# Optimization experiments

Measured on AMD Instinct MI355X. Metric: run time of the kernel, lower is better.

Reference implementation:

```python
import jax, jax.numpy as jnp
import numpy as np

N_NODES = 50000
N_EDGES = 1_600_000
DIMS = [3, 4096, 1024, 256, 64, 16]  # conv1..conv5 in/out widths


def setup_inputs() -> dict:
    key = jax.random.key(0)
    ks = jax.random.split(key, 2 + 2 * 6)
    x = jax.random.normal(ks[0], (N_NODES, DIMS[0]), jnp.float32)
    edge_index = jax.random.randint(ks[1], (2, N_EDGES), 0, N_NODES, jnp.int64)
    inp = {"x": x, "edge_index": edge_index}
    # GCNConv weights (lin has no bias fused; bias added after aggregation)
    for i in range(5):
        fi, fo = DIMS[i], DIMS[i + 1]
        inp[f"W{i+1}"] = jax.random.normal(ks[2 + 2 * i], (fi, fo), jnp.float32) / np.float32(np.sqrt(fi))
        inp[f"b{i+1}"] = jnp.zeros((fo,), jnp.float32)
    # final Linear(num_classes, 3)
    inp["Wl"] = jax.random.normal(ks[12], (DIMS[5], 3), jnp.float32) / np.float32(np.sqrt(DIMS[5]))
    inp["bl"] = jnp.zeros((3,), jnp.float32)
    return inp


def _gcn_layer(x, W, b, src, dst, dinv):
    """GCNConv: h = XW; out = D^-1/2 (A+I) D^-1/2 h + b (self-loops included)."""
    h = x @ W  # [N, out]
    norm = dinv[src] * dinv[dst]  # [E]
    agg = jax.ops.segment_sum(h[src] * norm[:, None], dst, num_segments=N_NODES)
    # self-loop term: norm_ii = dinv[i]^2
    return agg + h * (dinv * dinv)[:, None] + b


def reference(x, edge_index, W1, b1, W2, b2, W3, b3, W4, b4, W5, b5, Wl, bl):
    src, dst = edge_index[0], edge_index[1]
    # degree with self-loops (edge weights = 1), computed on target nodes
    deg = jax.ops.segment_sum(jnp.ones((N_EDGES,), x.dtype), dst, num_segments=N_NODES) + 1.0
    dinv = jax.lax.rsqrt(deg)
    h = _gcn_layer(x, W1, b1, src, dst, dinv)
    h = jax.nn.relu(h)  # dropout = identity in eval
    h = _gcn_layer(h, W2, b2, src, dst, dinv)
    h = jax.nn.relu(h)
    h = _gcn_layer(h, W3, b3, src, dst, dinv)
    h = jax.nn.relu(h)
    h = _gcn_layer(h, W4, b4, src, dst, dinv)
    h = jax.nn.relu(h)
    h = _gcn_layer(h, W5, b5, src, dst, dinv)
    # scatter_mean with broadcast index [0] -> global mean pool to [1, C]
    pooled = jnp.mean(h, axis=0, keepdims=True)
    return pooled @ Wl + bl  # [1, 3]
```

## Files before the change

### kernel.cpp

```cpp
#include <hip/hip_runtime.h>
#include <stdint.h>

#define NN 50000
#define NE 1600000

typedef _Float16 f16;
typedef __attribute__((ext_vector_type(8))) _Float16 h8;
typedef __attribute__((ext_vector_type(4))) _Float16 h4v;
typedef __attribute__((ext_vector_type(4))) float f32x4;
typedef __attribute__((ext_vector_type(2))) float f32x2;

union PackU { unsigned int u; f16 h[2]; };
union Pack4 { uint2 v; f16 h[4]; };

__device__ __forceinline__ void storev(float* p, float v) { *p = v; }
__device__ __forceinline__ void storev(f16* p, float v) { *p = (f16)v; }

__device__ __forceinline__ unsigned char f2fp8(float v) {
    int pk = __builtin_amdgcn_cvt_pk_fp8_f32(v, v, 0, false);
    return (unsigned char)(pk & 0xff);
}

__global__ __launch_bounds__(256) void zero_int_kernel(int* __restrict__ p, int n) {
    int i = blockIdx.x * 256 + threadIdx.x;
    if (i < n) p[i] = 0;
}

__global__ __launch_bounds__(256) void count_kernel(const int* __restrict__ dst,
                                                    int* __restrict__ deg, int nE) {
    int e = blockIdx.x * 256 + threadIdx.x;
    if (e < nE) atomicAdd(&deg[dst[e]], 1);
}

__global__ __launch_bounds__(256) void dinv_kernel(const int* __restrict__ deg,
                                                   float* __restrict__ dinv, int n) {
    int i = blockIdx.x * 256 + threadIdx.x;
    if (i < n) dinv[i] = rsqrtf((float)deg[i] + 1.0f);
}

__global__ __launch_bounds__(256) void scan1_kernel(const int* __restrict__ cnt,
                                                    int* __restrict__ rs,
                                                    int* __restrict__ bsum, int n) {
    __shared__ int sm[256];
    int b = blockIdx.x, t = threadIdx.x, i = b * 256 + t;
    int v = (i < n) ? cnt[i] : 0;
    sm[t] = v;
    __syncthreads();
    for (int off = 1; off < 256; off <<= 1) {
        int x = 0;
        if (t >= off) x = sm[t - off];
        __syncthreads();
        if (t >= off) sm[t] += x;
        __syncthreads();
    }
    if (i < n) rs[i] = sm[t] - v;
    if (t == 255) bsum[b] = sm[255];
}

__global__ __launch_bounds__(256) void scan2_kernel(int* __restrict__ bsum,
                                                    int* __restrict__ rs, int nb, int n) {
    __shared__ int sm[256];
    int t = threadIdx.x;
    int v = (t < nb) ? bsum[t] : 0;
    sm[t] = v;
    __syncthreads();
    for (int off = 1; off < 256; off <<= 1) {
        int x = 0;
        if (t >= off) x = sm[t - off];
        __syncthreads();
        if (t >= off) sm[t] += x;
        __syncthreads();
    }
    if (t < nb) bsum[t] = sm[t] - v;
    if (t == 255) rs[n] = sm[255];
}

__global__ __launch_bounds__(256) void scan3_kernel(int* __restrict__ rs,
                                                    const int* __restrict__ bsum, int n) {
    int i = blockIdx.x * 256 + threadIdx.x;
    if (i < n) rs[i] += bsum[blockIdx.x];
}

__global__ __launch_bounds__(256) void fill_kernel(const int* __restrict__ src,
                                                   const int* __restrict__ dst,
                                                   const int* __restrict__ rs,
                                                   int* __restrict__ cur,
                                                   int* __restrict__ csr, int nE) {
    int e = blockIdx.x * 256 + threadIdx.x;
    if (e < nE) {
        int d = dst[e];
        int p = rs[d] + atomicAdd(&cur[d], 1);
        csr[p] = src[e];
    }
}

__global__ __launch_bounds__(256) void pack_w1_kernel(const float* __restrict__ W1,
                                                      const float* __restrict__ b1,
                                                      float* __restrict__ w1p) {
    int k = blockIdx.x * 256 + threadIdx.x;
    if (k < 4096) {
        w1p[k * 4 + 0] = W1[k];
        w1p[k * 4 + 1] = W1[4096 + k];
        w1p[k * 4 + 2] = W1[8192 + k];
        w1p[k * 4 + 3] = b1[k];
    }
}

__global__ __launch_bounds__(256) void tconv_kernel(const float* __restrict__ W,
                                                    f16* __restrict__ Wt,
                                                    int K, int N) {
    __shared__ float tile[32][33];
    int kb = blockIdx.y * 32, nb = blockIdx.x * 32;
    int tx = threadIdx.x & 31, ty = threadIdx.x >> 5;
    for (int r = ty; r < 32; r += 8)
        tile[r][tx] = W[(size_t)(kb + r) * N + nb + tx];
    __syncthreads();
    for (int r = ty; r < 32; r += 8)
        Wt[(size_t)(nb + r) * K + kb + tx] = (f16)tile[tx][r];
}

template <int F, int TPN, bool RELU, bool BIAS, typename OutT>
__global__ __launch_bounds__(256) void agg_kernel(const float* __restrict__ t,
                                                  const float* __restrict__ dinv,
                                                  const int* __restrict__ rs,
                                                  const int* __restrict__ csr,
                                                  const float* __restrict__ bias,
                                                  OutT* __restrict__ out, int out_ld,
                                                  int nNodes) {
    constexpr int NPB = 256 / TPN;
    constexpr int C   = F / TPN;
    static_assert(TPN * C == F, "F must be TPN*C");
    int node = blockIdx.x * NPB + (int)threadIdx.x / TPN;
    if (node >= nNodes) return;
    int lane = (int)threadIdx.x % TPN;

    float acc[C];
#pragma unroll
    for (int c = 0; c < C; ++c) acc[c] = 0.f;

    int e0 = rs[node], e1 = rs[node + 1];
    for (int e = e0; e < e1; ++e) {
        int s = csr[e];
        float w = dinv[s];
        const float* tr = t + (size_t)s * F;
#pragma unroll
        for (int c = 0; c < C; ++c) acc[c] += w * tr[lane + c * TPN];
    }
    float di = dinv[node];
    const float* ti = t + (size_t)node * F;
    OutT* oi = out + (size_t)node * out_ld;
#pragma unroll
    for (int c = 0; c < C; ++c) {
        int col = lane + c * TPN;
        float v = di * acc[c] + di * di * ti[col];
        if (BIAS) v += bias[col];
        if (RELU) v = fmaxf(v, 0.f);
        storev(oi + col, v);
    }
}

template <bool RELU>
__global__ __launch_bounds__(256) void agg_fp8_256(const unsigned char* __restrict__ t,
                                                   int in_ld,
                                                   const float* __restrict__ dinv,
                                                   const int* __restrict__ rs,
                                                   const int* __restrict__ csr,
                                                   const float* __restrict__ bias,
                                                   f16* __restrict__ out,
                                                   int out_ld, int nNodes) {
    int node = blockIdx.x * 4 + ((int)threadIdx.x >> 6);
    if (node >= nNodes) return;
    int lane = (int)threadIdx.x & 63;

    float acc0 = 0.f, acc1 = 0.f, acc2 = 0.f, acc3 = 0.f;
    int e0 = rs[node], e1 = rs[node + 1];
    int e = e0;
    for (; e + 1 < e1; e += 2) {
        int s0 = csr[e], s1 = csr[e + 1];
        float w0 = dinv[s0], w1 = dinv[s1];
        unsigned int u0 = ((const unsigned int*)(t + (size_t)s0 * in_ld))[lane];
        unsigned int u1 = ((const unsigned int*)(t + (size_t)s1 * in_ld))[lane];
        f32x2 l0 = __builtin_amdgcn_cvt_pk_f32_fp8((int)u0, false);
        f32x2 h0 = __builtin_amdgcn_cvt_pk_f32_fp8((int)u0, true);
        f32x2 l1 = __builtin_amdgcn_cvt_pk_f32_fp8((int)u1, false);
        f32x2 h1 = __builtin_amdgcn_cvt_pk_f32_fp8((int)u1, true);
        acc0 += w0 * l0.x + w1 * l1.x;
        acc1 += w0 * l0.y + w1 * l1.y;
        acc2 += w0 * h0.x + w1 * h1.x;
        acc3 += w0 * h0.y + w1 * h1.y;
    }
    if (e < e1) {
        int s0 = csr[e];
        float w0 = dinv[s0];
        unsigned int u0 = ((const unsigned int*)(t + (size_t)s0 * in_ld))[lane];
        f32x2 l0 = __builtin_amdgcn_cvt_pk_f32_fp8((int)u0, false);
        f32x2 h0 = __builtin_amdgcn_cvt_pk_f32_fp8((int)u0, true);
        acc0 += w0 * l0.x;
        acc1 += w0 * l0.y;
        acc2 += w0 * h0.x;
        acc3 += w0 * h0.y;
    }
    float di = dinv[node], di2 = di * di;
    unsigned int us = ((const unsigned int*)(t + (size_t)node * in_ld))[lane];
    f32x2 sl = __builtin_amdgcn_cvt_pk_f32_fp8((int)us, false);
    f32x2 sh = __builtin_amdgcn_cvt_pk_f32_fp8((int)us, true);
    float4 b = *(const float4*)(bias + 4 * lane);
    float v0 = di * acc0 + di2 * sl.x + b.x;
    float v1 = di * acc1 + di2 * sl.y + b.y;
    float v2 = di * acc2 + di2 * sh.x + b.z;
    float v3 = di * acc3 + di2 * sh.y + b.w;
    if (RELU) {
        v0 = fmaxf(v0, 0.f); v1 = fmaxf(v1, 0.f);
        v2 = fmaxf(v2, 0.f); v3 = fmaxf(v3, 0.f);
    }
    Pack4 pk;
    pk.h[0] = (f16)v0; pk.h[1] = (f16)v1; pk.h[2] = (f16)v2; pk.h[3] = (f16)v3;
    *(uint2*)(out + (size_t)node * out_ld + 4 * lane) = pk.v;
}

#define LDSTR 40

__global__ __launch_bounds__(512, 4) void gemm12_mfma4(const float* __restrict__ aggx,
                                                       const float* __restrict__ w1p,
                                                       const f16* __restrict__ Bt,
                                                       unsigned char* __restrict__ t2) {
    __shared__ f16 As[128 * LDSTR] __attribute__((aligned(16)));
    __shared__ f16 Bs[256 * LDSTR] __attribute__((aligned(16)));
    int tid = threadIdx.x;
    int m0  = blockIdx.x * 128;
    int n0c = blockIdx.y * 256;

    int mg = tid >> 3;
    int kg = tid & 7;
    float a0[2], a1[2], a2[2];
#pragma unroll
    for (int j = 0; j < 2; ++j) {
        int gm = m0 + mg * 2 + j;
        if (gm < NN) {
            a0[j] = aggx[gm * 3 + 0];
            a1[j] = aggx[gm * 3 + 1];
            a2[j] = aggx[gm * 3 + 2];
        } else {
            a0[j] = a1[j] = a2[j] = 0.f;
        }
    }

    int brow = tid >> 1;
    int bkof = (tid & 1) * 16;
    const f16* bbase = Bt + (size_t)(n0c + brow) * 4096 + bkof;

    int lane   = tid & 63;
    int wv     = tid >> 6;
    int wm     = (wv >> 2) * 64;
    int wn     = (wv & 3) * 64;
    int fr_m   = lane & 15;
    int khalf8 = (lane >> 4) * 8;

    h8 pb0 = *(const h8*)(bbase);
    h8 pb1 = *(const h8*)(bbase + 8);

    f32x4 acc[4][4];
#pragma unroll
    for (int i = 0; i < 4; ++i)
#pragma unroll
        for (int j = 0; j < 4; ++j) acc[i][j] = (f32x4){0.f, 0.f, 0.f, 0.f};

    for (int k0 = 0; k0 < 4096; k0 += 32) {
        int kb = k0 + kg * 4;
        float4 wk0 = *(const float4*)(w1p + (size_t)(kb + 0) * 4);
        float4 wk1 = *(const float4*)(w1p + (size_t)(kb + 1) * 4);
        float4 wk2 = *(const float4*)(w1p + (size_t)(kb + 2) * 4);
        float4 wk3 = *(const float4*)(w1p + (size_t)(kb + 3) * 4);
#pragma unroll
        for (int j = 0; j < 2; ++j) {
            float h0 = fmaxf(a0[j] * wk0.x + a1[j] * wk0.y + a2[j] * wk0.z + wk0.w, 0.f);
            float h1 = fmaxf(a0[j] * wk1.x + a1[j] * wk1.y + a2[j] * wk1.z + wk1.w, 0.f);
            float h2 = fmaxf(a0[j] * wk2.x + a1[j] * wk2.y + a2[j] * wk2.z + wk2.w, 0.f);
            float h3 = fmaxf(a0[j] * wk3.x + a1[j] * wk3.y + a2[j] * wk3.z + wk3.w, 0.f);
            Pack4 pk;
            pk.h[0] = (f16)h0; pk.h[1] = (f16)h1; pk.h[2] = (f16)h2; pk.h[3] = (f16)h3;
            *(uint2*)(&As[(mg * 2 + j) * LDSTR + kg * 4]) = pk.v;
        }
        *(h8*)(&Bs[brow * LDSTR + bkof]) = pb0;
        *(h8*)(&Bs[brow * LDSTR + bkof + 8]) = pb1;
        __syncthreads();

        int kn = k0 + 32;
        if (kn < 4096) {
            pb0 = *(const h8*)(bbase + kn);
            pb1 = *(const h8*)(bbase + kn + 8);
        }

        h8 af[4];
#pragma unroll
        for (int mt = 0; mt < 4; ++mt)
            af[mt] = *(const h8*)(&As[(wm + mt * 16 + fr_m) * LDSTR + khalf8]);
#pragma unroll
        for (int nt = 0; nt < 4; ++nt) {
            h8 bf = *(const h8*)(&Bs[(wn + nt * 16 + fr_m) * LDSTR + khalf8]);
#pragma unroll
            for (int mt = 0; mt < 4; ++mt)
                acc[mt][nt] = __builtin_amdgcn_mfma_f32_16x16x32_f16(af[mt], bf, acc[mt][nt], 0, 0, 0);
        }
        __syncthreads();
    }

#pragma unroll
    for (int mt = 0; mt < 4; ++mt) {
#pragma unroll
        for (int reg = 0; reg < 4; ++reg) {
            int gm = m0 + wm + mt * 16 + (lane >> 4) * 4 + reg;
            if (gm < NN) {
                unsigned char* orow = t2 + (size_t)gm * 1024 + n0c + wn + fr_m;
#pragma unroll
                for (int nt = 0; nt < 4; ++nt)
                    orow[nt * 16] = f2fp8(acc[mt][nt][reg]);
            }
        }
    }
}

__global__ __launch_bounds__(256) void gemm_mfma(const f16* __restrict__ A, int lda,
                                                 const f16* __restrict__ Bt, int K,
                                                 unsigned char* __restrict__ C, int ldc,
                                                 int M) {
    __shared__ f16 As[128 * LDSTR] __attribute__((aligned(16)));
    __shared__ f16 Bs[128 * LDSTR] __attribute__((aligned(16)));
    int tid = threadIdx.x;
    int m0 = blockIdx.y * 128;
    int n0 = blockIdx.x * 128;

    int row = tid >> 1;
    int kof = (tid & 1) * 16;
    int am  = m0 + row;
    if (am > M - 1) am = M - 1;

    int lane   = tid & 63;
    int wv     = tid >> 6;
    int fr_m   = lane & 15;
    int khalf8 = (lane >> 4) * 8;

    const f16* abase = A + (size_t)am * lda + kof;
    const f16* bbase = Bt + (size_t)(n0 + row) * K + kof;

    h8 pa0 = *(const h8*)(abase);
    h8 pa1 = *(const h8*)(abase + 8);
    h8 pb0 = *(const h8*)(bbase);
    h8 pb1 = *(const h8*)(bbase + 8);

    f32x4 acc[2][8];
#pragma unroll
    for (int i = 0; i < 2; ++i)
#pragma unroll
        for (int j = 0; j < 8; ++j) acc[i][j] = (f32x4){0.f, 0.f, 0.f, 0.f};

    for (int k0 = 0; k0 < K; k0 += 32) {
        *(h8*)(&As[row * LDSTR + kof]) = pa0;
        *(h8*)(&As[row * LDSTR + kof + 8]) = pa1;
        *(h8*)(&Bs[row * LDSTR + kof]) = pb0;
        *(h8*)(&Bs[row * LDSTR + kof + 8]) = pb1;
        __syncthreads();

        int kn = k0 + 32;
        if (kn < K) {
            pa0 = *(const h8*)(abase + kn);
            pa1 = *(const h8*)(abase + kn + 8);
            pb0 = *(const h8*)(bbase + kn);
            pb1 = *(const h8*)(bbase + kn + 8);
        }

        h8 af0 = *(const h8*)(&As[(wv * 32 + fr_m) * LDSTR + khalf8]);
        h8 af1 = *(const h8*)(&As[(wv * 32 + 16 + fr_m) * LDSTR + khalf8]);
#pragma unroll
        for (int nt = 0; nt < 8; ++nt) {
            h8 bf = *(const h8*)(&Bs[(nt * 16 + fr_m) * LDSTR + khalf8]);
            acc[0][nt] = __builtin_amdgcn_mfma_f32_16x16x32_f16(af0, bf, acc[0][nt], 0, 0, 0);
            acc[1][nt] = __builtin_amdgcn_mfma_f32_16x16x32_f16(af1, bf, acc[1][nt], 0, 0, 0);
        }
        __syncthreads();
    }

#pragma unroll
    for (int mt = 0; mt < 2; ++mt) {
#pragma unroll
        for (int reg = 0; reg < 4; ++reg) {
            int gm = m0 + wv * 32 + mt * 16 + (lane >> 4) * 4 + reg;
            if (gm < M) {
                unsigned char* orow = C + (size_t)gm * ldc + n0 + fr_m;
#pragma unroll
                for (int nt = 0; nt < 8; ++nt)
                    orow[nt * 16] = f2fp8(acc[mt][nt][reg]);
            }
        }
    }
}

#define BM 64
#define BN 64
#define BKS 16
__global__ __launch_bounds__(256) void gemm_f16A_kernel(const f16* __restrict__ A,
                                                        const float* __restrict__ B,
                                                        float* __restrict__ C,
                                                        int M, int K, int N) {
    __shared__ float As[BKS][BM + 4];
    __shared__ float Bs[BKS][BN + 4];
    int tid = threadIdx.x;
    int tx = tid & 15;
    int ty = tid >> 4;
    int m0 = blockIdx.y * BM;
    int n0 = blockIdx.x * BN;

    float acc[4][4];
#pragma unroll
    for (int i = 0; i < 4; ++i)
#pragma unroll
        for (int j = 0; j < 4; ++j) acc[i][j] = 0.f;

    int lmA = tid >> 2;
    int lkA = (tid & 3) * 4;
    int lkB = tid >> 4;
    int lnB = (tid & 15) * 4;

    for (int k0 = 0; k0 < K; k0 += BKS) {
        int gm = m0 + lmA;
        if (gm > M - 1) gm = M - 1;
        h4v av = *(const h4v*)(A + (size_t)gm * K + k0 + lkA);
        As[lkA + 0][lmA] = (float)av.x;
        As[lkA + 1][lmA] = (float)av.y;
        As[lkA + 2][lmA] = (float)av.z;
        As[lkA + 3][lmA] = (float)av.w;
        float4 bv = *reinterpret_cast<const float4*>(B + (size_t)(k0 + lkB) * N + n0 + lnB);
        *reinterpret_cast<float4*>(&Bs[lkB][lnB]) = bv;
        __syncthreads();

#pragma unroll
        for (int k = 0; k < BKS; ++k) {
            float4 a4 = *reinterpret_cast<const float4*>(&As[k][ty * 4]);
            float4 b4 = *reinterpret_cast<const float4*>(&Bs[k][tx * 4]);
            float a[4] = {a4.x, a4.y, a4.z, a4.w};
            float b[4] = {b4.x, b4.y, b4.z, b4.w};
#pragma unroll
            for (int i = 0; i < 4; ++i)
#pragma unroll
                for (int j = 0; j < 4; ++j) acc[i][j] += a[i] * b[j];
        }
        __syncthreads();
    }

#pragma unroll
    for (int i = 0; i < 4; ++i) {
        int m = m0 + ty * 4 + i;
        if (m < M) {
            float4 o = make_float4(acc[i][0], acc[i][1], acc[i][2], acc[i][3]);
            *reinterpret_cast<float4*>(C + (size_t)m * N + n0 + tx * 4) = o;
        }
    }
}

__global__ __launch_bounds__(256) void gemm5_kernel(const f16* __restrict__ h4,
                                                    const float* __restrict__ W5,
                                                    float* __restrict__ t5, int nNodes) {
    int idx = blockIdx.x * 256 + threadIdx.x;
    int i = idx >> 4, j = idx & 15;
    if (i >= nNodes) return;
    const f16* a = h4 + (size_t)i * 64;
    float s = 0.f;
#pragma unroll
    for (int k = 0; k < 64; ++k) s += (float)a[k] * W5[k * 16 + j];
    t5[idx] = s;
}

__global__ __launch_bounds__(256) void pool_kernel(const float* __restrict__ h5,
                                                   float* __restrict__ pool) {
    __shared__ float red[256];
    int c = blockIdx.x;
    float s = 0.f;
    for (int i = threadIdx.x; i < NN; i += 256) s += h5[(size_t)i * 16 + c];
    red[threadIdx.x] = s;
    __syncthreads();
    for (int off = 128; off > 0; off >>= 1) {
        if ((int)threadIdx.x < off) red[threadIdx.x] += red[threadIdx.x + off];
        __syncthreads();
    }
    if (threadIdx.x == 0) pool[c] = red[0];
}

__global__ void final_kernel(const float* __restrict__ pool, const float* __restrict__ Wl,
                             const float* __restrict__ bl, float* __restrict__ out) {
    int j = threadIdx.x;
    if (j < 3) {
        float s = 0.f;
#pragma unroll
        for (int c = 0; c < 16; ++c) s += pool[c] * Wl[c * 3 + j];
        out[j] = s * (1.0f / (float)NN) + bl[j];
    }
}

extern "C" void kernel_launch(void* const* d_in, const int* in_sizes, int n_in,
                              void* d_out, int out_size, void* d_ws, size_t ws_size,
                              hipStream_t stream) {
    (void)in_sizes; (void)n_in; (void)out_size; (void)ws_size;

    const float* x  = (const float*)d_in[0];
    const int*   ei = (const int*)d_in[1];
    const float* W1 = (const float*)d_in[2];
    const float* b1 = (const float*)d_in[3];
    const float* W2 = (const float*)d_in[4];
    const float* b2 = (const float*)d_in[5];
    const float* W3 = (const float*)d_in[6];
    const float* b3 = (const float*)d_in[7];
    const float* W4 = (const float*)d_in[8];
    const float* b4 = (const float*)d_in[9];
    const float* W5 = (const float*)d_in[10];
    const float* b5 = (const float*)d_in[11];
    const float* Wl = (const float*)d_in[12];
    const float* bl = (const float*)d_in[13];
    float* out = (float*)d_out;

    const int* srcp = ei;
    const int* dstp = ei + NE;

    char* p = (char*)d_ws;
    auto carve = [&](size_t bytes) {
        char* r = p;
        p += (bytes + 255) & ~(size_t)255;
        return r;
    };
    int*   deg  = (int*)carve(NN * 4);
    int*   cur  = (int*)carve(NN * 4);
    int*   rs   = (int*)carve((NN + 1) * 4);
    int*   bsum = (int*)carve(256 * 4);
    int*   csr  = (int*)carve((size_t)NE * 4);
    float* dinv = (float*)carve(NN * 4);
    float* aggx = (float*)carve((size_t)NN * 3 * 4);
    float* pool = (float*)carve(16 * 4);
    float* w1p  = (float*)carve((size_t)4096 * 4 * 4);
    f16*   w2t  = (f16*)carve((size_t)1024 * 4096 * 2);
    f16*   w3t  = (f16*)carve((size_t)256 * 1024 * 2);
    unsigned char* tbuf = (unsigned char*)carve((size_t)NN * 1024);
    f16*   h2   = (f16*)carve((size_t)NN * 1024 * 2);
    f16*   h3   = (f16*)carve((size_t)NN * 256 * 2);
    f16*   h4   = (f16*)carve((size_t)NN * 64 * 2);
    float* h5   = (float*)carve((size_t)NN * 16 * 4);
    float* tf32 = (float*)tbuf;

    const int NB = (NN + 255) / 256;

    zero_int_kernel<<<NB, 256, 0, stream>>>(deg, NN);
    zero_int_kernel<<<NB, 256, 0, stream>>>(cur, NN);
    count_kernel<<<(NE + 255) / 256, 256, 0, stream>>>(dstp, deg, NE);
    dinv_kernel<<<NB, 256, 0, stream>>>(deg, dinv, NN);
    scan1_kernel<<<NB, 256, 0, stream>>>(deg, rs, bsum, NN);
    scan2_kernel<<<1, 256, 0, stream>>>(bsum, rs, NB, NN);
    scan3_kernel<<<NB, 256, 0, stream>>>(rs, bsum, NN);
    fill_kernel<<<(NE + 255) / 256, 256, 0, stream>>>(srcp, dstp, rs, cur, csr, NE);

    pack_w1_kernel<<<16, 256, 0, stream>>>(W1, b1, w1p);
    tconv_kernel<<<dim3(1024 / 32, 4096 / 32), 256, 0, stream>>>(W2, w2t, 4096, 1024);
    tconv_kernel<<<dim3(256 / 32, 1024 / 32), 256, 0, stream>>>(W3, w3t, 1024, 256);

    agg_kernel<3, 1, false, false, float><<<NB, 256, 0, stream>>>(
        x, dinv, rs, csr, nullptr, aggx, 3, NN);

    const int MB2 = (NN + 127) / 128;

    gemm12_mfma4<<<dim3(MB2, 4), 512, 0, stream>>>(aggx, w1p, w2t, tbuf);
    for (int c = 0; c < 4; ++c) {
        int c0 = c * 256;
        agg_fp8_256<true><<<(NN + 3) / 4, 256, 0, stream>>>(
            tbuf + c0, 1024, dinv, rs, csr, b2 + c0, h2 + c0, 1024, NN);
    }

    gemm_mfma<<<dim3(2, MB2), 256, 0, stream>>>(
        h2, 1024, w3t, 1024, tbuf, 256, NN);
    agg_fp8_256<true><<<(NN + 3) / 4, 256, 0, stream>>>(
        tbuf, 256, dinv, rs, csr, b3, h3, 256, NN);

    gemm_f16A_kernel<<<dim3(1, (NN + BM - 1) / BM), 256, 0, stream>>>(
        h3, W4, tf32, NN, 256, 64);
    agg_kernel<64, 64, true, true, f16><<<(NN + 3) / 4, 256, 0, stream>>>(
        tf32, dinv, rs, csr, b4, h4, 64, NN);

    gemm5_kernel<<<(NN * 16 + 255) / 256, 256, 0, stream>>>(h4, W5, tf32, NN);
    agg_kernel<16, 16, false, true, float><<<(NN + 15) / 16, 256, 0, stream>>>(
        tf32, dinv, rs, csr, b5, h5, 16, NN);

    pool_kernel<<<16, 256, 0, stream>>>(h5, pool);
    final_kernel<<<1, 64, 0, stream>>>(pool, Wl, bl, out);
}
```

Before: 1.782 ms.

## Load B fragments directly from global memory and double-buffer A tile in fused GEMM

The fused layer-1/layer-2 GEMM no longer stages the W2 tile in shared memory. Each wave reads its B fragments straight from global memory into registers, relying on L2 and L1 to serve reuse across the two M-waves. The A tile is double-buffered in shared memory, which removes one of the two barriers per K step. This cuts LDS traffic and synchronisation, at the cost of more global/L2 load traffic and exposed load latency with no prefetch.

```diff
diff --git a/kernel.cpp b/kernel.cpp
--- a/kernel.cpp
+++ b/kernel.cpp
@@ -220,12 +220,11 @@
 
 #define LDSTR 40
 
-__global__ __launch_bounds__(512, 4) void gemm12_mfma4(const float* __restrict__ aggx,
+__global__ __launch_bounds__(512, 4) void gemm12_mfma5(const float* __restrict__ aggx,
                                                        const float* __restrict__ w1p,
                                                        const f16* __restrict__ Bt,
                                                        unsigned char* __restrict__ t2) {
-    __shared__ f16 As[128 * LDSTR] __attribute__((aligned(16)));
-    __shared__ f16 Bs[256 * LDSTR] __attribute__((aligned(16)));
+    __shared__ f16 As[2][128 * LDSTR] __attribute__((aligned(16)));
     int tid = threadIdx.x;
     int m0  = blockIdx.x * 128;
     int n0c = blockIdx.y * 256;
@@ -245,10 +244,6 @@
         }
     }
 
-    int brow = tid >> 1;
-    int bkof = (tid & 1) * 16;
-    const f16* bbase = Bt + (size_t)(n0c + brow) * 4096 + bkof;
-
     int lane   = tid & 63;
     int wv     = tid >> 6;
     int wm     = (wv >> 2) * 64;
@@ -256,8 +251,7 @@
     int fr_m   = lane & 15;
     int khalf8 = (lane >> 4) * 8;
 
-    h8 pb0 = *(const h8*)(bbase);
-    h8 pb1 = *(const h8*)(bbase + 8);
+    const f16* bb = Bt + (size_t)(n0c + wn + fr_m) * 4096 + khalf8;
 
     f32x4 acc[4][4];
 #pragma unroll
@@ -266,6 +260,7 @@
         for (int j = 0; j < 4; ++j) acc[i][j] = (f32x4){0.f, 0.f, 0.f, 0.f};
 
     for (int k0 = 0; k0 < 4096; k0 += 32) {
+        int buf = (k0 >> 5) & 1;
         int kb = k0 + kg * 4;
         float4 wk0 = *(const float4*)(w1p + (size_t)(kb + 0) * 4);
         float4 wk1 = *(const float4*)(w1p + (size_t)(kb + 1) * 4);
@@ -279,30 +274,26 @@
             float h3 = fmaxf(a0[j] * wk3.x + a1[j] * wk3.y + a2[j] * wk3.z + wk3.w, 0.f);
             Pack4 pk;
             pk.h[0] = (f16)h0; pk.h[1] = (f16)h1; pk.h[2] = (f16)h2; pk.h[3] = (f16)h3;
-            *(uint2*)(&As[(mg * 2 + j) * LDSTR + kg * 4]) = pk.v;
-        }
-        *(h8*)(&Bs[brow * LDSTR + bkof]) = pb0;
-        *(h8*)(&Bs[brow * LDSTR + bkof + 8]) = pb1;
-        __syncthreads();
-
-        int kn = k0 + 32;
-        if (kn < 4096) {
-            pb0 = *(const h8*)(bbase + kn);
-            pb1 = *(const h8*)(bbase + kn + 8);
-        }
+            *(uint2*)(&As[buf][(mg * 2 + j) * LDSTR + kg * 4]) = pk.v;
+        }
+        __syncthreads();
+
+        h8 bf[4];
+#pragma unroll
+        for (int nt = 0; nt < 4; ++nt)
+            bf[nt] = *(const h8*)(bb + (size_t)nt * 16 * 4096 + k0);
 
         h8 af[4];
 #pragma unroll
         for (int mt = 0; mt < 4; ++mt)
-            af[mt] = *(const h8*)(&As[(wm + mt * 16 + fr_m) * LDSTR + khalf8]);
+            af[mt] = *(const h8*)(&As[buf][(wm + mt * 16 + fr_m) * LDSTR + khalf8]);
+
 #pragma unroll
         for (int nt = 0; nt < 4; ++nt) {
-            h8 bf = *(const h8*)(&Bs[(wn + nt * 16 + fr_m) * LDSTR + khalf8]);
 #pragma unroll
             for (int mt = 0; mt < 4; ++mt)
-                acc[mt][nt] = __builtin_amdgcn_mfma_f32_16x16x32_f16(af[mt], bf, acc[mt][nt], 0, 0, 0);
-        }
-        __syncthreads();
+                acc[mt][nt] = __builtin_amdgcn_mfma_f32_16x16x32_f16(af[mt], bf[nt], acc[mt][nt], 0, 0, 0);
+        }
     }
 
 #pragma unroll
@@ -564,7 +555,7 @@
 
     const int MB2 = (NN + 127) / 128;
 
-    gemm12_mfma4<<<dim3(MB2, 4), 512, 0, stream>>>(aggx, w1p, w2t, tbuf);
+    gemm12_mfma5<<<dim3(MB2, 4), 512, 0, stream>>>(aggx, w1p, w2t, tbuf);
     for (int c = 0; c < 4; ++c) {
         int c0 = c * 256;
         agg_fp8_256<true><<<(NN + 3) / 4, 256, 0, stream>>>(
```

Result: slower. 2.322 ms (+30.3%).
